# Kernel tuning notes

Measured on AMD Instinct MI355X. Metric: run time of the kernel, lower is better.

The kernel has to match this reference:

```python
import jax, jax.numpy as jnp
import numpy as np
import math

E = 768      # embed_size
H = 12       # heads
D = E // H   # head_dim = 64
MAXLEN = 512
N = 8        # batch
L = 512      # seq_len (q_len == k_len)


def _sinusoid_table():
    # (2*MAXLEN-1, E) sinusoidal table, sin at even dims, cos at odd dims
    pos = jnp.arange(2 * MAXLEN - 1, dtype=jnp.float32)[:, None]
    div = jnp.exp(jnp.arange(0, E, 2, dtype=jnp.float32) * (-math.log(10000.0) / E))
    ang = pos * div  # (2M-1, E/2)
    return jnp.stack([jnp.sin(ang), jnp.cos(ang)], axis=-1).reshape(2 * MAXLEN - 1, E)


def setup_inputs() -> dict:
    key = jax.random.key(0)
    ks = jax.random.split(key, 16)
    sc = 0.02
    return {
        "values": jax.random.normal(ks[0], (N, L, E), jnp.float32),
        "keys": jax.random.normal(ks[1], (N, L, E), jnp.float32),
        "query": jax.random.normal(ks[2], (N, L, E), jnp.float32),
        "Wq": jax.random.normal(ks[3], (E, E), jnp.float32) * sc,
        "bq": jax.random.normal(ks[4], (E,), jnp.float32) * sc,
        "Wk": jax.random.normal(ks[5], (E, E), jnp.float32) * sc,
        "bk": jax.random.normal(ks[6], (E,), jnp.float32) * sc,
        "Wv": jax.random.normal(ks[7], (E, E), jnp.float32) * sc,
        "bv": jax.random.normal(ks[8], (E,), jnp.float32) * sc,
        "Wo": jax.random.normal(ks[9], (E, E), jnp.float32) * sc,
        "bo": jax.random.normal(ks[10], (E,), jnp.float32) * sc,
        "Wpos": jax.random.normal(ks[11], (E, E), jnp.float32) * sc,
        "bpos": jax.random.normal(ks[12], (E,), jnp.float32) * sc,
        "r_w_bias": jax.random.normal(ks[13], (H, D), jnp.float32),
        "r_r_bias": jax.random.normal(ks[14], (H, D), jnp.float32),
    }


def _rel_shift(x):
    # Faithful to the torch code: pad one row on q dim, shape-preserving view,
    # drop first row -> identity as written.
    xp = jnp.pad(x, ((0, 0), (0, 0), (1, 0), (0, 0)))
    return xp[:, :, 1:, :]


def reference(values, keys, query, Wq, bq, Wk, bk, Wv, bv, Wo, bo, Wpos, bpos, r_w_bias, r_r_bias):
    pe = _sinusoid_table()  # (2M-1, E)
    r = jnp.arange(L)
    idx = jnp.clip(r[:, None] - r[None, :] + (MAXLEN - 1), 0, 2 * MAXLEN - 2)  # (L, L)
    rel = pe[idx] @ Wpos + bpos                       # (L, L, E)
    rel = rel.reshape(L, L, H, D).transpose(2, 0, 1, 3)  # (H, L, L, D)

    q = (query @ Wq + bq).reshape(N, L, H, D)
    k = (keys @ Wk + bk).reshape(N, L, H, D)
    v = (values @ Wv + bv).reshape(N, L, H, D)

    ac = jnp.einsum('nqhd,nkhd->nhqk', q + r_w_bias[None, None], k)
    bd = jnp.einsum('nqhd,hqkd->nhqk', q + r_r_bias[None, None], rel)
    bd = _rel_shift(bd)

    scores = (ac + bd) / math.sqrt(D)
    attn = jax.nn.softmax(scores, axis=-1)
    out = jnp.einsum('nhqk,nkhd->nqhd', attn, v).reshape(N, L, E)
    return out @ Wo + bo
```

## Files before the change

kernel.cpp:

```cpp
#include <hip/hip_runtime.h>

typedef unsigned short u16;
typedef unsigned int u32;
typedef __bf16 bf16x8 __attribute__((ext_vector_type(8)));
typedef float f32x4 __attribute__((ext_vector_type(4)));

#define EMB 768
#define NH 12
#define HD 64
#define SEQ 512
#define NB 8
#define NLROWS 4096
#define PEROWS 1024

__device__ __forceinline__ float b2f(u16 u) {
    return __uint_as_float(((u32)u) << 16);
}
__device__ __forceinline__ u16 f2b(float f) {
    u32 x = __float_as_uint(f);
    u32 r = x + 0x7fffu + ((x >> 16) & 1u);
    return (u16)(r >> 16);
}
__device__ __forceinline__ u32 pack2(float a, float b) {
    return (u32)f2b(a) | ((u32)f2b(b) << 16);
}
__device__ __forceinline__ u32 cvtpk(float lo, float hi) {
    u32 r;
    asm("v_cvt_pk_bf16_f32 %0, %1, %2" : "=v"(r) : "v"(lo), "v"(hi));
    return r;
}
__device__ __forceinline__ void cfence() { asm volatile("" ::: "memory"); }
__device__ __forceinline__ void gl_lds16(const u16* g, u16* l) {
    __builtin_amdgcn_global_load_lds((const __attribute__((address_space(1))) u32*)g,
                                     (__attribute__((address_space(3))) u32*)l, 16, 0, 0);
}

__global__ __launch_bounds__(256) void prep(
        const float* __restrict__ Wq, const float* __restrict__ Wk, const float* __restrict__ Wv,
        const float* __restrict__ Wo, const float* __restrict__ Wpos,
        u16* __restrict__ Wt, u16* __restrict__ pe,
        const float* __restrict__ q, const float* __restrict__ k, const float* __restrict__ v,
        u16* __restrict__ qc, u16* __restrict__ kc, u16* __restrict__ vc) {
    __shared__ u16 tile[32][33];
    int b = blockIdx.x;
    int tid = threadIdx.x;
    if (b < 2880) {
        int m = b / 576, r = b % 576;
        const float* src = (m == 0) ? Wq : (m == 1) ? Wk : (m == 2) ? Wv : (m == 3) ? Wo : Wpos;
        u16* dst = Wt + (size_t)m * EMB * EMB;
        int bx = (r % 24) * 32, by = (r / 24) * 32;
        int tx = tid & 31, ty = tid >> 5;
#pragma unroll
        for (int i = 0; i < 32; i += 8)
            tile[ty + i][tx] = f2b(src[(size_t)(by + ty + i) * EMB + bx + tx]);
        __syncthreads();
        int c2 = (tid & 15) * 2, rw = tid >> 4;
#pragma unroll
        for (int i = 0; i < 32; i += 16) {
            int row = rw + i;
            u32 val = (u32)tile[c2][row] | ((u32)tile[c2 + 1][row] << 16);
            *(u32*)&dst[(size_t)(bx + row) * EMB + by + c2] = val;
        }
    } else if (b < 3904) {
        int pos = b - 2880;
        int p2 = pos > 1022 ? 1022 : pos;
#pragma unroll
        for (int j = 0; j < 3; j++) {
            int col = tid + j * 256;
            int i = col >> 1;
            float ang = (float)p2 * __expf(-0.023985261384f * (float)i);
            float val = (col & 1) ? __cosf(ang) : __sinf(ang);
            pe[(size_t)pos * EMB + col] = f2b(val);
        }
    } else {
        int idx = b - 3904;
        int w = idx / 1536, bx = idx % 1536;
        const float* s = (w == 0) ? q : (w == 1) ? k : v;
        u16* d = (w == 0) ? qc : (w == 1) ? kc : vc;
        size_t i = ((size_t)bx * 256 + tid) * 8;
        float4 f0 = *(const float4*)(s + i);
        float4 f1 = *(const float4*)(s + i + 4);
        uint4 o;
        o.x = pack2(f0.x, f0.y); o.y = pack2(f0.z, f0.w);
        o.z = pack2(f1.x, f1.y); o.w = pack2(f1.z, f1.w);
        *(uint4*)(d + i) = o;
    }
}

template <int BM, int BN, int NZ, bool OUTF32>
__global__ __launch_bounds__(256, 4) void gemm_k(
        const u16* A0, const u16* A1, const u16* A2, const u16* A3,
        const u16* W0, const u16* W1, const u16* W2, const u16* W3,
        const float* f0, const float* f1, const float* f2, const float* f3,
        void* C0, void* C1, void* C2, void* C3) {
    constexpr int RT = BM / 32;
    constexpr int CT = BN / 32;
    __shared__ __align__(16) u16 As[BM * 64];
    __shared__ __align__(16) u16 Bs[BN * 64];
    int z = (NZ > 1) ? blockIdx.z : 0;
    if (NZ > 1 && z == 3 && blockIdx.x >= PEROWS / BM) return;
    const u16* A = (z == 0) ? A0 : (z == 1) ? A1 : (z == 2) ? A2 : A3;
    const u16* Bt = (z == 0) ? W0 : (z == 1) ? W1 : (z == 2) ? W2 : W3;
    const float* bias = (z == 0) ? f0 : (z == 1) ? f1 : (z == 2) ? f2 : f3;
    void* Cv = (z == 0) ? C0 : (z == 1) ? C1 : (z == 2) ? C2 : C3;
    bool vtout = (NZ > 1) && (z == 2);

    int tid = threadIdx.x;
    int wave = tid >> 6, lane = tid & 63;
    int lrow = lane & 15, lq = lane >> 4;
    int lr8 = lane >> 3, lb = lane & 7;
    int m0 = blockIdx.x * BM, n0 = blockIdx.y * BN;
    int wr = (wave >> 1) * (BM / 2), wc = (wave & 1) * (BN / 2);
    const u16* Abase = A + (size_t)m0 * EMB + (size_t)(lb ^ lr8) * 8;
    const u16* Bbase = Bt + (size_t)n0 * EMB + (size_t)(lb ^ lr8) * 8;
    f32x4 acc[RT][CT] = {};

    for (int k0 = 0; k0 < EMB; k0 += 64) {
        __syncthreads();
#pragma unroll
        for (int j = 0; j < BM / 32; j++) {
            int row = j * 32 + wave * 8 + lr8;
            gl_lds16(Abase + (size_t)row * EMB + k0, &As[(j * 32 + wave * 8) * 64]);
        }
#pragma unroll
        for (int j = 0; j < BN / 32; j++) {
            int row = j * 32 + wave * 8 + lr8;
            gl_lds16(Bbase + (size_t)row * EMB + k0, &Bs[(j * 32 + wave * 8) * 64]);
        }
        __syncthreads();
#pragma unroll
        for (int ks = 0; ks < 2; ks++) {
            int pb = (ks * 4 + lq) ^ (lrow & 7);
            bf16x8 bfr[CT];
#pragma unroll
            for (int ct = 0; ct < CT; ct++)
                bfr[ct] = *(const bf16x8*)&Bs[(wc + ct * 16 + lrow) * 64 + pb * 8];
#pragma unroll
            for (int rt = 0; rt < RT; rt++) {
                bf16x8 afr = *(const bf16x8*)&As[(wr + rt * 16 + lrow) * 64 + pb * 8];
#pragma unroll
                for (int ct = 0; ct < CT; ct++)
                    acc[rt][ct] = __builtin_amdgcn_mfma_f32_16x16x32_bf16(afr, bfr[ct], acc[rt][ct], 0, 0, 0);
            }
        }
    }
#pragma unroll
    for (int rt = 0; rt < RT; rt++) {
#pragma unroll
        for (int ct = 0; ct < CT; ct++) {
            int col = n0 + wc + ct * 16 + lrow;
            float bvv = bias[col];
            int mrow = m0 + wr + rt * 16 + lq * 4;
            if (vtout) {
                int nb = mrow >> 9, kvl = mrow & 511;
                int hh = col >> 6, dl = col & 63;
                ushort4 pk;
                pk.x = f2b(acc[rt][ct][0] + bvv);
                pk.y = f2b(acc[rt][ct][1] + bvv);
                pk.z = f2b(acc[rt][ct][2] + bvv);
                pk.w = f2b(acc[rt][ct][3] + bvv);
                *(ushort4*)((u16*)Cv + (((size_t)(nb * NH + hh) * HD + dl) << 9) + kvl) = pk;
            } else if (OUTF32) {
#pragma unroll
                for (int r = 0; r < 4; r++)
                    ((float*)Cv)[(size_t)(mrow + r) * EMB + col] = acc[rt][ct][r] + bvv;
            } else {
#pragma unroll
                for (int r = 0; r < 4; r++)
                    ((u16*)Cv)[(size_t)(mrow + r) * EMB + col] = f2b(acc[rt][ct][r] + bvv);
            }
        }
    }
}

__global__ __launch_bounds__(256, 3) void attn_rpe(
        const u16* __restrict__ Qb, const u16* __restrict__ Kb, const u16* __restrict__ Vtg,
        const u16* __restrict__ Rb, const float* __restrict__ rwb, const float* __restrict__ rrb,
        u16* __restrict__ Ctx) {
    __shared__ __align__(16) u16 Ks[64 * 64];
    __shared__ __align__(16) u16 Vt[64 * 64];
    __shared__ __align__(16) u16 Rs[128 * 64];
    __shared__ __align__(16) u16 PsPb[4 * 1664];

    int q0 = blockIdx.x * 64;
    int h = blockIdx.y;
    int n = blockIdx.z;
    int tid = threadIdx.x;
    int wave = tid >> 6, lane = tid & 63;
    int lrow = lane & 15, lq = lane >> 4;
    int lr8 = lane >> 3, lb = lane & 7;
    int swz = (lb ^ lr8) * 8;
    u16* psd = &PsPb[wave * 1664];

    bf16x8 aw[2], ar[2];
    {
        const u16* qrow = Qb + ((size_t)(n * SEQ + q0 + wave * 16 + lrow)) * EMB + h * HD;
#pragma unroll
        for (int ks = 0; ks < 2; ks++) {
            int c = ks * 32 + lq * 8;
            uint4 qv = *(const uint4*)(qrow + c);
            float4 w0 = *(const float4*)(rwb + h * HD + c);
            float4 w1 = *(const float4*)(rwb + h * HD + c + 4);
            float4 r0 = *(const float4*)(rrb + h * HD + c);
            float4 r1 = *(const float4*)(rrb + h * HD + c + 4);
            union { uint4 u; u16 s[8]; } qu; qu.u = qv;
            union { uint4 u; bf16x8 v; } ww, rr;
            ww.u.x = pack2(b2f(qu.s[0]) + w0.x, b2f(qu.s[1]) + w0.y);
            ww.u.y = pack2(b2f(qu.s[2]) + w0.z, b2f(qu.s[3]) + w0.w);
            ww.u.z = pack2(b2f(qu.s[4]) + w1.x, b2f(qu.s[5]) + w1.y);
            ww.u.w = pack2(b2f(qu.s[6]) + w1.z, b2f(qu.s[7]) + w1.w);
            rr.u.x = pack2(b2f(qu.s[0]) + r0.x, b2f(qu.s[1]) + r0.y);
            rr.u.y = pack2(b2f(qu.s[2]) + r0.z, b2f(qu.s[3]) + r0.w);
            rr.u.z = pack2(b2f(qu.s[4]) + r1.x, b2f(qu.s[5]) + r1.y);
            rr.u.w = pack2(b2f(qu.s[6]) + r1.z, b2f(qu.s[7]) + r1.w);
            aw[ks] = ww.v;
            ar[ks] = rr.v;
        }
    }

    auto stage_chunk = [&](int cc) {
#pragma unroll
        for (int j = 0; j < 2; j++) {
            int row = j * 32 + wave * 8 + lr8;
            gl_lds16(Kb + ((size_t)(n * SEQ + cc + row)) * EMB + h * HD + swz,
                     &Ks[(j * 32 + wave * 8) * 64]);
        }
#pragma unroll
        for (int j = 0; j < 2; j++) {
            int row = j * 32 + wave * 8 + lr8;
            gl_lds16(Vtg + (((size_t)(n * NH + h) * HD + row) << 9) + cc + swz,
                     &Vt[(j * 32 + wave * 8) * 64]);
        }
#pragma unroll
        for (int j = 0; j < 4; j++) {
            int row = j * 32 + wave * 8 + lr8;
            gl_lds16(Rb + (size_t)(q0 - cc + 448 + row) * EMB + h * HD + swz,
                     &Rs[(j * 32 + wave * 8) * 64]);
        }
    };

    float lsum = 0.f;
    f32x4 acco[4] = {};

    stage_chunk(0);
    for (int c0 = 0; c0 < SEQ; c0 += 64) {
        __syncthreads();

        f32x4 sacc[4] = {};
        f32x4 pacc[5] = {};
        bf16x8 vf[2][4];
#pragma unroll
        for (int ks = 0; ks < 2; ks++) {
            int pb = (ks * 4 + lq) ^ (lrow & 7);
#pragma unroll
            for (int ct = 0; ct < 4; ct++) {
                bf16x8 bk = *(const bf16x8*)&Ks[(ct * 16 + lrow) * 64 + pb * 8];
                sacc[ct] = __builtin_amdgcn_mfma_f32_16x16x32_bf16(bk, aw[ks], sacc[ct], 0, 0, 0);
            }
#pragma unroll
            for (int jj = 0; jj < 5; jj++) {
                bf16x8 br = *(const bf16x8*)&Rs[((wave + jj) * 16 + lrow) * 64 + pb * 8];
                pacc[jj] = __builtin_amdgcn_mfma_f32_16x16x32_bf16(ar[ks], br, pacc[jj], 0, 0, 0);
            }
#pragma unroll
            for (int dt = 0; dt < 4; dt++)
                vf[ks][dt] = *(const bf16x8*)&Vt[(dt * 16 + lrow) * 64 + pb * 8];
        }
        __syncthreads();
        if (c0 + 64 < SEQ) stage_chunk(c0 + 64);

#pragma unroll
        for (int jj = 0; jj < 5; jj++) {
            uint2 pk2;
            pk2.x = cvtpk(pacc[jj][0], pacc[jj][1]);
            pk2.y = cvtpk(pacc[jj][2], pacc[jj][3]);
            *(uint2*)&psd[(jj * 16 + lrow) * 20 + lq * 4] = pk2;
        }
        cfence();

        float bd[4][4];
#pragma unroll
        for (int ct = 0; ct < 4; ct++)
#pragma unroll
            for (int r = 0; r < 4; r++) {
                int jwin = lrow - (ct * 16 + lq * 4 + r) + 63;
                bd[ct][r] = b2f(psd[jwin * 20 + lrow]);
            }
        cfence();

#pragma unroll
        for (int ct = 0; ct < 4; ct++) {
            float p0 = exp2f((sacc[ct][0] + bd[ct][0]) * 0.18033688011f);
            float p1 = exp2f((sacc[ct][1] + bd[ct][1]) * 0.18033688011f);
            float p2 = exp2f((sacc[ct][2] + bd[ct][2]) * 0.18033688011f);
            float p3 = exp2f((sacc[ct][3] + bd[ct][3]) * 0.18033688011f);
            lsum += (p0 + p1) + (p2 + p3);
            uint2 pk2;
            pk2.x = cvtpk(p0, p1);
            pk2.y = cvtpk(p2, p3);
            *(uint2*)&psd[lrow * 72 + ct * 16 + lq * 4] = pk2;
        }
        cfence();

#pragma unroll
        for (int ks = 0; ks < 2; ks++) {
            bf16x8 pf = *(const bf16x8*)&psd[lrow * 72 + ks * 32 + lq * 8];
#pragma unroll
            for (int dt = 0; dt < 4; dt++)
                acco[dt] = __builtin_amdgcn_mfma_f32_16x16x32_bf16(vf[ks][dt], pf, acco[dt], 0, 0, 0);
        }
    }

    lsum += __shfl_xor(lsum, 16);
    lsum += __shfl_xor(lsum, 32);
    float inv = 1.0f / lsum;
    int q = q0 + wave * 16 + lrow;
#pragma unroll
    for (int dt = 0; dt < 4; dt++) {
        ushort4 pk;
        pk.x = f2b(acco[dt][0] * inv);
        pk.y = f2b(acco[dt][1] * inv);
        pk.z = f2b(acco[dt][2] * inv);
        pk.w = f2b(acco[dt][3] * inv);
        *(ushort4*)&Ctx[((size_t)(n * SEQ + q)) * EMB + h * HD + dt * 16 + lq * 4] = pk;
    }
}

extern "C" void kernel_launch(void* const* d_in, const int* in_sizes, int n_in,
                              void* d_out, int out_size, void* d_ws, size_t ws_size,
                              hipStream_t stream) {
    const float* values = (const float*)d_in[0];
    const float* keys   = (const float*)d_in[1];
    const float* query  = (const float*)d_in[2];
    const float* Wq = (const float*)d_in[3];
    const float* bq = (const float*)d_in[4];
    const float* Wk = (const float*)d_in[5];
    const float* bk = (const float*)d_in[6];
    const float* Wv = (const float*)d_in[7];
    const float* bv = (const float*)d_in[8];
    const float* Wo = (const float*)d_in[9];
    const float* bo = (const float*)d_in[10];
    const float* Wpos = (const float*)d_in[11];
    const float* bpos = (const float*)d_in[12];
    const float* rwb = (const float*)d_in[13];
    const float* rrb = (const float*)d_in[14];
    float* out = (float*)d_out;

    u16* ws = (u16*)d_ws;
    size_t off = 0;
    u16* Wt = ws;            off += (size_t)5 * EMB * EMB;
    u16* pe = ws + off;      off += (size_t)PEROWS * EMB;
    u16* Rb = ws + off;      off += (size_t)PEROWS * EMB;
    u16* qc = ws + off;      off += (size_t)NLROWS * EMB;
    u16* kc = ws + off;      off += (size_t)NLROWS * EMB;
    u16* vc = ws + off;      off += (size_t)NLROWS * EMB;
    u16* Qp = ws + off;      off += (size_t)NLROWS * EMB;
    u16* Kp = ws + off;      off += (size_t)NLROWS * EMB;
    u16* Vtg = ws + off;     off += (size_t)NLROWS * EMB;
    u16* Cx = qc;

    prep<<<dim3(8512), dim3(256), 0, stream>>>(Wq, Wk, Wv, Wo, Wpos, Wt, pe,
                                               query, keys, values, qc, kc, vc);

    gemm_k<128, 96, 4, false><<<dim3(32, 8, 4), dim3(256), 0, stream>>>(
        qc, kc, vc, pe,
        Wt, Wt + (size_t)1 * EMB * EMB, Wt + (size_t)2 * EMB * EMB, Wt + (size_t)4 * EMB * EMB,
        bq, bk, bv, bpos,
        Qp, Kp, Vtg, Rb);

    attn_rpe<<<dim3(8, NH, NB), dim3(256), 0, stream>>>(Qp, Kp, Vtg, Rb, rwb, rrb, Cx);

    gemm_k<64, 64, 1, true><<<dim3(64, 12), dim3(256), 0, stream>>>(
        Cx, Cx, Cx, Cx,
        Wt + (size_t)3 * EMB * EMB, Wt + (size_t)3 * EMB * EMB,
        Wt + (size_t)3 * EMB * EMB, Wt + (size_t)3 * EMB * EMB,
        bo, bo, bo, bo,
        out, out, out, out);
}
```

Before: 174.6 us.

## Reuse overlapping relative-position rows via ring buffer and raise MFMA wave priority

The 128-row relative-position tile in LDS becomes a circular buffer. Each iteration now fetches only the 64 new rows that the next key chunk needs and reuses the 64 that overlap, which halves the R global-to-LDS traffic per step. Row indices are wrapped modulo 128. s_setprio is also raised around the MFMA sections so waves in matrix math are favoured by the scheduler. The cost is extra index arithmetic, and the prefetch has to line up exactly with the sliding window.

```diff
diff --git a/kernel.cpp b/kernel.cpp
--- a/kernel.cpp
+++ b/kernel.cpp
@@ -218,7 +218,7 @@
         }
     }
 
-    auto stage_chunk = [&](int cc) {
+    auto stage_kv = [&](int cc) {
 #pragma unroll
         for (int j = 0; j < 2; j++) {
             int row = j * 32 + wave * 8 + lr8;
@@ -231,24 +231,30 @@
             gl_lds16(Vtg + (((size_t)(n * NH + h) * HD + row) << 9) + cc + swz,
                      &Vt[(j * 32 + wave * 8) * 64]);
         }
-#pragma unroll
-        for (int j = 0; j < 4; j++) {
-            int row = j * 32 + wave * 8 + lr8;
-            gl_lds16(Rb + (size_t)(q0 - cc + 448 + row) * EMB + h * HD + swz,
-                     &Rs[(j * 32 + wave * 8) * 64]);
-        }
     };
 
     float lsum = 0.f;
     f32x4 acco[4] = {};
 
-    stage_chunk(0);
+    stage_kv(0);
+    {
+        int base0 = (q0 + 448) & 127;
+#pragma unroll
+        for (int j = 0; j < 4; j++) {
+            int nr = j * 32 + wave * 8;
+            gl_lds16(Rb + (size_t)(q0 + 448 + nr + lr8) * EMB + h * HD + swz,
+                     &Rs[((base0 + nr) & 127) * 64]);
+        }
+    }
+
     for (int c0 = 0; c0 < SEQ; c0 += 64) {
         __syncthreads();
 
+        int rbase = (q0 + 448 - c0) & 127;
         f32x4 sacc[4] = {};
         f32x4 pacc[5] = {};
         bf16x8 vf[2][4];
+        __builtin_amdgcn_s_setprio(1);
 #pragma unroll
         for (int ks = 0; ks < 2; ks++) {
             int pb = (ks * 4 + lq) ^ (lrow & 7);
@@ -259,15 +265,27 @@
             }
 #pragma unroll
             for (int jj = 0; jj < 5; jj++) {
-                bf16x8 br = *(const bf16x8*)&Rs[((wave + jj) * 16 + lrow) * 64 + pb * 8];
+                int rrow = (rbase + (wave + jj) * 16 + lrow) & 127;
+                bf16x8 br = *(const bf16x8*)&Rs[rrow * 64 + pb * 8];
                 pacc[jj] = __builtin_amdgcn_mfma_f32_16x16x32_bf16(ar[ks], br, pacc[jj], 0, 0, 0);
             }
 #pragma unroll
             for (int dt = 0; dt < 4; dt++)
                 vf[ks][dt] = *(const bf16x8*)&Vt[(dt * 16 + lrow) * 64 + pb * 8];
         }
-        __syncthreads();
-        if (c0 + 64 < SEQ) stage_chunk(c0 + 64);
+        __builtin_amdgcn_s_setprio(0);
+        __syncthreads();
+        if (c0 + 64 < SEQ) {
+            stage_kv(c0 + 64);
+            int gb = q0 - c0 + 384;
+            int sb = gb & 127;
+#pragma unroll
+            for (int j = 0; j < 2; j++) {
+                int nr = j * 32 + wave * 8;
+                gl_lds16(Rb + (size_t)(gb + nr + lr8) * EMB + h * HD + swz,
+                         &Rs[((sb + nr) & 127) * 64]);
+            }
+        }
 
 #pragma unroll
         for (int jj = 0; jj < 5; jj++) {
@@ -302,6 +320,7 @@
         }
         cfence();
 
+        __builtin_amdgcn_s_setprio(1);
 #pragma unroll
         for (int ks = 0; ks < 2; ks++) {
             bf16x8 pf = *(const bf16x8*)&psd[lrow * 72 + ks * 32 + lq * 8];
@@ -309,6 +328,7 @@
             for (int dt = 0; dt < 4; dt++)
                 acco[dt] = __builtin_amdgcn_mfma_f32_16x16x32_bf16(vf[ks][dt], pf, acco[dt], 0, 0, 0);
         }
+        __builtin_amdgcn_s_setprio(0);
     }
 
     lsum += __shfl_xor(lsum, 16);
```

Result: slower. 178.7 us (+2.4%).
